# Optimization experiments

Hardware: AMD Instinct MI355X
Metric: run time of the kernel (lower is better)

Reference implementation:

```python
import jax, jax.numpy as jnp
import numpy as np

WS, OWS, NH = 16, 24, 2          # window size, overlap window size (=int(16*0.5)+16), num heads
PAD = (OWS - WS) // 2            # unfold padding = 4


def conv2d(x, w, b):
    kh, kw = w.shape[2], w.shape[3]
    out = jax.lax.conv_general_dilated(x, w, (1, 1), [(kh // 2, kh // 2), (kw // 2, kw // 2)],
                                       dimension_numbers=('NCHW', 'OIHW', 'NCHW'))
    return out + b[None, :, None, None]


def layer_norm(x, g, b, eps=1e-5):
    m = x.mean(-1, keepdims=True)
    v = ((x - m) ** 2).mean(-1, keepdims=True)
    return (x - m) * jax.lax.rsqrt(v + eps) * g + b


def stem(depth, cw1, cb1, cw2, cb2, cw3, cb3, cw4, cb4, in_g, in_b):
    # BasicConv(1->8,k3,relu) -> (8->16,k1,relu) -> (16->16,k3,relu) -> (16->32,k1) -> InstanceNorm2d(32,affine)
    y = jax.nn.relu(conv2d(depth, cw1, cb1))
    y = jax.nn.relu(conv2d(y, cw2, cb2))
    y = jax.nn.relu(conv2d(y, cw3, cb3))
    y = conv2d(y, cw4, cb4)
    m = y.mean((2, 3), keepdims=True)
    v = ((y - m) ** 2).mean((2, 3), keepdims=True)
    return (y - m) * jax.lax.rsqrt(v + 1e-5) * in_g[None, :, None, None] + in_b[None, :, None, None]


def ocab(xq, ykv, rpi, n1g, n1b, wq, bq, wkv, bkv, rpb, wp, bp, n2g, n2b, mw1, mb1, mw2, mb2):
    # Overlapping cross-attention block (HAT-style OCAB, cross variant: q from xq, kv from ykv).
    b, c, h, w = xq.shape
    x = xq.transpose(0, 2, 3, 1)   # b h w c
    y = ykv.transpose(0, 2, 3, 1)
    shortcut = x
    q = layer_norm(x, n1g, n1b) @ wq + bq          # b h w c
    kv = layer_norm(y, n1g, n1b) @ wkv + bkv       # b h w 2c
    nhw, nww = h // WS, w // WS
    # non-overlapping query windows: (b*nw, WS*WS, c)
    qw = q.reshape(b, nhw, WS, nww, WS, c).transpose(0, 1, 3, 2, 4, 5).reshape(b * nhw * nww, WS * WS, c)
    # overlapping kv windows via unfold (patch channel order = (channel, kh, kw), same as torch unfold)
    patches = jax.lax.conv_general_dilated_patches(kv.transpose(0, 3, 1, 2), (OWS, OWS), (WS, WS),
                                                   [(PAD, PAD), (PAD, PAD)])  # b, 2c*OWS*OWS, nhw, nww
    patches = patches.reshape(b, 2, c, OWS * OWS, nhw * nww).transpose(1, 0, 4, 3, 2).reshape(2, b * nhw * nww, OWS * OWS, c)
    k, v = patches[0], patches[1]
    d = c // NH
    qh = qw.reshape(-1, WS * WS, NH, d).transpose(0, 2, 1, 3) * (d ** -0.5)
    kh = k.reshape(-1, OWS * OWS, NH, d).transpose(0, 2, 1, 3)
    vh = v.reshape(-1, OWS * OWS, NH, d).transpose(0, 2, 1, 3)
    attn = jnp.einsum('whqd,whkd->whqk', qh, kh)
    attn = attn + rpb[rpi].transpose(2, 0, 1)[None]  # rel-pos bias -> [1, NH, WS*WS, OWS*OWS]
    attn = jax.nn.softmax(attn, axis=-1)
    out = jnp.einsum('whqk,whkd->whqd', attn, vh).transpose(0, 2, 1, 3).reshape(-1, WS * WS, c)
    # window reverse
    out = out.reshape(b, nhw, nww, WS, WS, c).transpose(0, 1, 3, 2, 4, 5).reshape(b, h, w, c)
    out = out @ wp + bp + shortcut
    out = out + (jax.nn.gelu(layer_norm(out, n2g, n2b) @ mw1 + mb1) @ mw2 + mb2)  # mlp_ratio=2
    return out.transpose(0, 3, 1, 2)


def setup_inputs():
    key = jax.random.key(0)
    ks = jax.random.split(key, 16)
    B, C, H, W = 1, 32, 256, 256
    s = 0.05
    return dict(
        x=jax.random.normal(ks[0], (B, C, H, W), jnp.float32),
        depth=jax.random.normal(ks[1], (B, 1, H, W), jnp.float32),
        rpi=jax.random.randint(ks[2], (WS * WS, OWS * OWS), 0, (WS + OWS - 1) ** 2),
        cw1=jax.random.normal(ks[3], (8, 1, 3, 3)) * s, cb1=jnp.zeros(8),
        cw2=jax.random.normal(ks[4], (16, 8, 1, 1)) * s, cb2=jnp.zeros(16),
        cw3=jax.random.normal(ks[5], (16, 16, 3, 3)) * s, cb3=jnp.zeros(16),
        cw4=jax.random.normal(ks[6], (32, 16, 1, 1)) * s, cb4=jnp.zeros(32),
        in_g=jnp.ones(32), in_b=jnp.zeros(32),
        n1g=jnp.ones(C), n1b=jnp.zeros(C),
        wq=jax.random.normal(ks[7], (C, C)) * s, bq=jnp.zeros(C),
        wkv=jax.random.normal(ks[8], (C, 2 * C)) * s, bkv=jnp.zeros(2 * C),
        rpb=jax.random.normal(ks[9], ((WS + OWS - 1) ** 2, NH)) * 0.02,
        wp=jax.random.normal(ks[10], (C, C)) * s, bp=jnp.zeros(C),
        n2g=jnp.ones(C), n2b=jnp.zeros(C),
        mw1=jax.random.normal(ks[11], (C, 2 * C)) * s, mb1=jnp.zeros(2 * C),
        mw2=jax.random.normal(ks[12], (2 * C, C)) * s, mb2=jnp.zeros(C),
    )


def reference(x, depth, rpi, cw1, cb1, cw2, cb2, cw3, cb3, cw4, cb4, in_g, in_b,
              n1g, n1b, wq, bq, wkv, bkv, rpb, wp, bp, n2g, n2b, mw1, mb1, mw2, mb2):
    f = stem(depth, cw1, cb1, cw2, cb2, cw3, cb3, cw4, cb4, in_g, in_b)
    a = (n1g, n1b, wq, bq, wkv, bkv, rpb, wp, bp, n2g, n2b, mw1, mb1, mw2, mb2)
    out1 = ocab(x, f, rpi, *a)   # shared OCAB weights, called twice with swapped roles
    out2 = ocab(f, x, rpi, *a)
    return out1 + out2 + x
```

## Files before the change

### kernel.cpp

```cpp
#include <hip/hip_runtime.h>
#include <hip/hip_bf16.h>

#define HW 65536
#define KPAD 584

typedef __attribute__((ext_vector_type(8))) short bf8;
typedef __attribute__((ext_vector_type(4))) float f4;

__device__ __forceinline__ unsigned short f2b(float x) {
  unsigned int u = __float_as_uint(x);
  unsigned int r = (u + 0x7fff + ((u >> 16) & 1)) >> 16;
  return (unsigned short)r;
}
__device__ __forceinline__ unsigned int pk2(float lo, float hi) {
  return (__float_as_uint(hi) & 0xffff0000u) | (__float_as_uint(lo) >> 16);
}

__device__ __forceinline__ void stem_front_body(
    int bx, int t, const float* __restrict__ depth,
    const float* __restrict__ cw1, const float* __restrict__ cb1,
    const float* __restrict__ cw2, const float* __restrict__ cb2,
    float* __restrict__ t2) {
  int p = bx * 256 + t;
  int y = p >> 8, x = p & 255;
  float in9[9];
#pragma unroll
  for (int ky = 0; ky < 3; ky++)
#pragma unroll
    for (int kx = 0; kx < 3; kx++) {
      int yy = y + ky - 1, xx = x + kx - 1;
      bool ok = ((unsigned)yy < 256u) && ((unsigned)xx < 256u);
      in9[ky*3+kx] = ok ? depth[yy*256+xx] : 0.f;
    }
  float t1[8];
#pragma unroll
  for (int o = 0; o < 8; o++) {
    float s = cb1[o];
#pragma unroll
    for (int i = 0; i < 9; i++) s += in9[i] * cw1[o*9+i];
    t1[o] = fmaxf(s, 0.f);
  }
#pragma unroll
  for (int o = 0; o < 16; o++) {
    float s = cb2[o];
#pragma unroll
    for (int ci = 0; ci < 8; ci++) s += t1[ci] * cw2[o*8+ci];
    t2[o*HW + p] = fmaxf(s, 0.f);
  }
}

__device__ __forceinline__ void bias_body(
    int bx, int t, const int* __restrict__ rpi,
    const float* __restrict__ rpb, float* __restrict__ biasT) {
  int idx = bx*256 + t;
  int hd = idx / 147456;
  int rem = idx - hd*147456;
  int qt = rem / 9216;
  int r2 = rem - qt*9216;
  int kb = r2 >> 6;
  int q16 = (r2 >> 2) & 15;
  int r = r2 & 3;
  int key = kb*4 + r;
  int qq = qt*16 + q16;
  biasT[idx] = rpb[rpi[qq*576 + key]*2 + hd] - 8.0f;
}

__device__ __forceinline__ void lnmm_body(
    int slab, int bx, int t,
    float* ws, float* gs, float* bs, float* b2s, float* as, float* bbs,
    const float* __restrict__ x, const float* __restrict__ t4,
    const float* __restrict__ part,
    const float* __restrict__ ig, const float* __restrict__ ib,
    const float* __restrict__ n1g, const float* __restrict__ n1b,
    const float* __restrict__ wq, const float* __restrict__ bq,
    const float* __restrict__ wkv, const float* __restrict__ bkv,
    float* q1, float* kv1, float* q2, float* kv2) {
  const float* src; const float* wm; const float* bo; float* dst;
  int wstride, coff; bool apply_in;
  switch (slab) {
    default:
    case 0: src=x;  wm=wq;  bo=bq;  dst=q1;         wstride=32; coff=0;  apply_in=false; break;
    case 1: src=t4; wm=wkv; bo=bkv; dst=kv1;        wstride=64; coff=0;  apply_in=true;  break;
    case 2: src=t4; wm=wkv; bo=bkv; dst=kv1+32*HW;  wstride=64; coff=32; apply_in=true;  break;
    case 3: src=t4; wm=wq;  bo=bq;  dst=q2;         wstride=32; coff=0;  apply_in=true;  break;
    case 4: src=x;  wm=wkv; bo=bkv; dst=kv2;        wstride=64; coff=0;  apply_in=false; break;
    case 5: src=x;  wm=wkv; bo=bkv; dst=kv2+32*HW;  wstride=64; coff=32; apply_in=false; break;
  }
  for (int i = t; i < 1024; i += 256) ws[i] = wm[(i>>5)*wstride + coff + (i&31)];
  if (t < 32) {
    gs[t] = n1g[t]; bs[t] = n1b[t]; b2s[t] = bo[coff+t];
    if (apply_in) {
      float s = 0.f, ss = 0.f;
#pragma unroll
      for (int k = 0; k < 16; k++) { s += part[t*16+k]; ss += part[512 + t*16+k]; }
      float m = s * (1.f/65536.f);
      float var = ss * (1.f/65536.f) - m*m;
      float a = rsqrtf(var + 1e-5f) * ig[t];
      as[t] = a; bbs[t] = ib[t] - m*a;
    }
  }
  __syncthreads();
  int p = bx*256 + t;
  float v[32]; float s = 0.f;
  if (apply_in) {
#pragma unroll
    for (int c = 0; c < 32; c++) { v[c] = src[c*HW+p]*as[c] + bbs[c]; s += v[c]; }
  } else {
#pragma unroll
    for (int c = 0; c < 32; c++) { v[c] = src[c*HW+p]; s += v[c]; }
  }
  float m = s * 0.03125f;
  float ss = 0.f;
#pragma unroll
  for (int c = 0; c < 32; c++) { float d = v[c]-m; ss += d*d; }
  float rs = rsqrtf(ss*0.03125f + 1e-5f);
  float acc[32];
#pragma unroll
  for (int j = 0; j < 32; j++) acc[j] = b2s[j];
#pragma unroll
  for (int c = 0; c < 32; c++) {
    float ln = (v[c]-m)*rs*gs[c] + bs[c];
    const float4* w4 = (const float4*)&ws[c*32];
#pragma unroll
    for (int j4 = 0; j4 < 8; j4++) {
      float4 w = w4[j4];
      acc[j4*4+0] += ln*w.x; acc[j4*4+1] += ln*w.y;
      acc[j4*4+2] += ln*w.z; acc[j4*4+3] += ln*w.w;
    }
  }
#pragma unroll
  for (int j = 0; j < 32; j++) dst[j*HW+p] = acc[j];
}

__global__ __launch_bounds__(256) void k_misc(
    const float* __restrict__ depth,
    const float* __restrict__ cw1, const float* __restrict__ cb1,
    const float* __restrict__ cw2, const float* __restrict__ cb2,
    float* __restrict__ t2,
    const int* __restrict__ rpi, const float* __restrict__ rpb, float* __restrict__ biasT,
    const float* __restrict__ x, const float* __restrict__ t4, const float* __restrict__ part,
    const float* __restrict__ ig, const float* __restrict__ ib,
    const float* __restrict__ n1g, const float* __restrict__ n1b,
    const float* __restrict__ wq, const float* __restrict__ bq,
    const float* __restrict__ wkv, const float* __restrict__ bkv,
    float* q1, float* kv1, float* q2, float* kv2) {
  __shared__ __align__(16) float ws[1024];
  __shared__ float gs[32], bs[32], b2s[32], as[32], bbs[32];
  int role = blockIdx.y, t = threadIdx.x, bx = blockIdx.x;
  if (role == 0) { if (bx < 256) stem_front_body(bx, t, depth, cw1, cb1, cw2, cb2, t2); return; }
  if (role == 1) { bias_body(bx, t, rpi, rpb, biasT); return; }
  if (bx >= 256) return;
  int slab = (role == 2) ? 0 : role + 1;
  lnmm_body(slab, bx, t, ws, gs, bs, b2s, as, bbs,
            x, t4, part, ig, ib, n1g, n1b, wq, bq, wkv, bkv, q1, kv1, q2, kv2);
}

__global__ __launch_bounds__(256) void k_lnmm3(
    const float* __restrict__ x, const float* __restrict__ t4, const float* __restrict__ part,
    const float* __restrict__ ig, const float* __restrict__ ib,
    const float* __restrict__ n1g, const float* __restrict__ n1b,
    const float* __restrict__ wq, const float* __restrict__ bq,
    const float* __restrict__ wkv, const float* __restrict__ bkv,
    float* q1, float* kv1, float* q2, float* kv2, int ybase) {
  __shared__ __align__(16) float ws[1024];
  __shared__ float gs[32], bs[32], b2s[32], as[32], bbs[32];
  lnmm_body(ybase + blockIdx.y, blockIdx.x, threadIdx.x, ws, gs, bs, b2s, as, bbs,
            x, t4, part, ig, ib, n1g, n1b, wq, bq, wkv, bkv, q1, kv1, q2, kv2);
}

__global__ __launch_bounds__(256) void k_conv3(
    const float* __restrict__ t2, const float* __restrict__ cw3,
    const float* __restrict__ cb3, float* __restrict__ t3) {
  int t = threadIdx.x;
  int p = blockIdx.x*256 + t;
  int og = blockIdx.y;
  int y = p >> 8, x = p & 255;
  float acc[4];
#pragma unroll
  for (int o = 0; o < 4; o++) acc[o] = cb3[og*4+o];
#pragma unroll 1
  for (int tap = 0; tap < 9; tap++) {
    int ky = tap/3 - 1, kx = tap - (tap/3)*3 - 1;
    int yy = y+ky, xx = x+kx;
    bool ok = ((unsigned)yy < 256u) && ((unsigned)xx < 256u);
    int pp = yy*256+xx;
#pragma unroll
    for (int ci = 0; ci < 16; ci++) {
      float v = ok ? t2[ci*HW+pp] : 0.f;
#pragma unroll
      for (int o = 0; o < 4; o++)
        acc[o] += v * cw3[(og*4+o)*144 + ci*9 + tap];
    }
  }
#pragma unroll
  for (int o = 0; o < 4; o++) t3[(og*4+o)*HW+p] = fmaxf(acc[o], 0.f);
}

__global__ __launch_bounds__(256) void k_conv4(
    const float* __restrict__ t3, const float* __restrict__ cw4,
    const float* __restrict__ cb4, float* __restrict__ t4) {
  int t = threadIdx.x;
  int p = blockIdx.x*256 + t;
  float v[16];
#pragma unroll
  for (int ci = 0; ci < 16; ci++) v[ci] = t3[ci*HW+p];
#pragma unroll
  for (int o = 0; o < 32; o++) {
    float s = cb4[o];
#pragma unroll
    for (int ci = 0; ci < 16; ci++) s += v[ci]*cw4[o*16+ci];
    t4[o*HW+p] = s;
  }
}

__global__ __launch_bounds__(256) void k_instats1(const float* __restrict__ t4,
                                                  float* __restrict__ part) {
  int c = blockIdx.x >> 4, seg = blockIdx.x & 15;
  const float4* src = (const float4*)(t4 + c*HW + seg*4096);
  float s = 0.f, ss = 0.f;
  for (int i = threadIdx.x; i < 1024; i += 256) {
    float4 v = src[i];
    s  += v.x + v.y + v.z + v.w;
    ss += v.x*v.x + v.y*v.y + v.z*v.z + v.w*v.w;
  }
#pragma unroll
  for (int off = 32; off > 0; off >>= 1) {
    s  += __shfl_down(s, off, 64);
    ss += __shfl_down(ss, off, 64);
  }
  __shared__ float sh[8];
  int wid = threadIdx.x >> 6;
  if ((threadIdx.x & 63) == 0) { sh[wid] = s; sh[4+wid] = ss; }
  __syncthreads();
  if (threadIdx.x == 0) {
    part[blockIdx.x]       = sh[0]+sh[1]+sh[2]+sh[3];
    part[512 + blockIdx.x] = sh[4]+sh[5]+sh[6]+sh[7];
  }
}

__global__ __launch_bounds__(256) void k_attn(
    const float* __restrict__ qA, const float* __restrict__ kvA, float* __restrict__ aoA,
    const float* __restrict__ qB, const float* __restrict__ kvB, float* __restrict__ aoB,
    const float* __restrict__ biasT) {
  __shared__ __align__(16) unsigned short Qs[256*16];
  __shared__ __align__(16) unsigned short Ks[576*16];
  __shared__ __align__(16) unsigned short Vt[16*KPAD];

  const float* q  = blockIdx.y ? qB  : qA;
  const float* kv = blockIdx.y ? kvB : kvA;
  float* ao       = blockIdx.y ? aoB : aoA;

  int wi = blockIdx.x >> 1, hd = blockIdx.x & 1;
  int wy = wi >> 4, wx = wi & 15;
  int t = threadIdx.x;
  int by = wy*16 - 4, bx = wx*16 - 4;
  int kbase = hd*16*HW, vbase = (32 + hd*16)*HW;

  {
    int qy = wy*16 + (t >> 4), qx = wx*16 + (t & 15);
    int p = qy*256 + qx;
    unsigned short tmp[16];
#pragma unroll
    for (int i = 0; i < 16; i++) tmp[i] = f2b(q[(hd*16+i)*HW + p] * 0.25f);
    *(uint4*)&Qs[t*16]     = *(uint4*)&tmp[0];
    *(uint4*)&Qs[t*16 + 8] = *(uint4*)&tmp[8];
  }
  for (int e = t; e < 576; e += 256) {
    int dy = e / 24, dx = e - dy*24;
    int yy = by + dy, xx = bx + dx;
    bool ok = ((unsigned)yy < 256u) && ((unsigned)xx < 256u);
    int pp = yy*256 + xx;
    int off = e & 31;
    int ppos = ((off & 12) << 1) + ((off >> 4) << 2) + (off & 3);
    int vcol = (e & ~31) + ppos;
    unsigned short tk[16];
#pragma unroll
    for (int i = 0; i < 16; i++) {
      float kvl = ok ? kv[kbase + i*HW + pp] : 0.f;
      float vvl = ok ? kv[vbase + i*HW + pp] : 0.f;
      tk[i] = f2b(kvl);
      Vt[i*KPAD + vcol] = f2b(vvl);
    }
    *(uint4*)&Ks[e*16]     = *(uint4*)&tk[0];
    *(uint4*)&Ks[e*16 + 8] = *(uint4*)&tk[8];
  }
  __syncthreads();

  int wave = t >> 6, lane = t & 63;
  int quad = lane >> 4, l16 = lane & 15;
  const bf8 zero8 = {0,0,0,0,0,0,0,0};

#pragma unroll 1
  for (int pp2 = 0; pp2 < 2; pp2++) {
    int qta = wave*4 + pp2*2, qtb = qta + 1;
    bf8 qfa = zero8, qfb = zero8;
    if (quad < 2) {
      qfa = *(const bf8*)&Qs[(qta*16 + l16)*16 + quad*8];
      qfb = *(const bf8*)&Qs[(qtb*16 + l16)*16 + quad*8];
    }
    f4 oa = {0.f,0.f,0.f,0.f}, ob = {0.f,0.f,0.f,0.f};
    float la = 0.f, lb = 0.f;
    const float* bba = biasT + (hd*16 + qta)*9216 + quad*64 + l16*4;
    const float* bbb = biasT + (hd*16 + qtb)*9216 + quad*64 + l16*4;
    f4 ba0 = *(const f4*)&bba[0];
    f4 ba1 = *(const f4*)&bba[256];
    f4 bb0 = *(const f4*)&bbb[0];
    f4 bb1 = *(const f4*)&bbb[256];

#pragma unroll 2
    for (int kt2 = 0; kt2 < 18; kt2++) {
      int k0 = kt2 * 32;
      f4 na0 = *(const f4*)&bba[(k0+32)*16];
      f4 na1 = *(const f4*)&bba[(k0+48)*16];
      f4 nb0 = *(const f4*)&bbb[(k0+32)*16];
      f4 nb1 = *(const f4*)&bbb[(k0+48)*16];
      bf8 kf0 = zero8, kf1 = zero8;
      if (quad < 2) {
        kf0 = *(const bf8*)&Ks[(k0 + l16)*16 + quad*8];
        kf1 = *(const bf8*)&Ks[(k0 + 16 + l16)*16 + quad*8];
      }
      f4 sa0 = __builtin_amdgcn_mfma_f32_16x16x32_bf16(kf0, qfa, ba0, 0, 0, 0);
      f4 sa1 = __builtin_amdgcn_mfma_f32_16x16x32_bf16(kf1, qfa, ba1, 0, 0, 0);
      f4 sb0 = __builtin_amdgcn_mfma_f32_16x16x32_bf16(kf0, qfb, bb0, 0, 0, 0);
      f4 sb1 = __builtin_amdgcn_mfma_f32_16x16x32_bf16(kf1, qfb, bb1, 0, 0, 0);
      float pa0[4], pa1[4], pb0[4], pb1[4];
#pragma unroll
      for (int r = 0; r < 4; r++) {
        pa0[r] = __expf(sa0[r]); pa1[r] = __expf(sa1[r]);
        pb0[r] = __expf(sb0[r]); pb1[r] = __expf(sb1[r]);
        la += pa0[r] + pa1[r];
        lb += pb0[r] + pb1[r];
      }
      union { unsigned int u[4]; bf8 v; } Pa, Pb;
      Pa.u[0] = pk2(pa0[0], pa0[1]); Pa.u[1] = pk2(pa0[2], pa0[3]);
      Pa.u[2] = pk2(pa1[0], pa1[1]); Pa.u[3] = pk2(pa1[2], pa1[3]);
      Pb.u[0] = pk2(pb0[0], pb0[1]); Pb.u[1] = pk2(pb0[2], pb0[3]);
      Pb.u[2] = pk2(pb1[0], pb1[1]); Pb.u[3] = pk2(pb1[2], pb1[3]);
      bf8 vf = *(const bf8*)&Vt[l16*KPAD + k0 + quad*8];
      oa = __builtin_amdgcn_mfma_f32_16x16x32_bf16(Pa.v, vf, oa, 0, 0, 0);
      ob = __builtin_amdgcn_mfma_f32_16x16x32_bf16(Pb.v, vf, ob, 0, 0, 0);
      ba0 = na0; ba1 = na1; bb0 = nb0; bb1 = nb1;
    }
    la += __shfl_xor(la, 16, 64); la += __shfl_xor(la, 32, 64);
    lb += __shfl_xor(lb, 16, 64); lb += __shfl_xor(lb, 32, 64);
#pragma unroll
    for (int r = 0; r < 4; r++) {
      float lva = __shfl(la, quad*4 + r, 64);
      float lvb = __shfl(lb, quad*4 + r, 64);
      int qwa = qta*16 + quad*4 + r;
      int qwb = qtb*16 + quad*4 + r;
      ao[(hd*16 + l16)*HW + (wy*16 + (qwa >> 4))*256 + wx*16 + (qwa & 15)] = oa[r] / lva;
      ao[(hd*16 + l16)*HW + (wy*16 + (qwb >> 4))*256 + wx*16 + (qwb & 15)] = ob[r] / lvb;
    }
  }
}

__global__ __launch_bounds__(256) void k_projmlp(
    const float* __restrict__ ao1, const float* __restrict__ ao2,
    const float* __restrict__ x, const float* __restrict__ t4,
    const float* __restrict__ part,
    const float* __restrict__ ig, const float* __restrict__ ib,
    const float* __restrict__ wp, const float* __restrict__ bp,
    const float* __restrict__ n2g, const float* __restrict__ n2b,
    const float* __restrict__ mw1, const float* __restrict__ mb1,
    const float* __restrict__ mw2, const float* __restrict__ mb2,
    float* __restrict__ o1, float* __restrict__ o2, int obase) {
  int oc = blockIdx.y + obase;
  const float* ao = oc ? ao2 : ao1;
  float* dst      = oc ? o2  : o1;
  __shared__ __align__(16) float wps[1024];
  __shared__ __align__(16) float w1s[2048];
  __shared__ __align__(16) float w2s[2048];
  __shared__ float bps[32], b1s[64], b2s[32], gs[32], bs[32], as[32], bbs[32];
  int t = threadIdx.x;
  for (int i = t; i < 1024; i += 256) wps[i] = wp[i];
  for (int i = t; i < 2048; i += 256) { w1s[i] = mw1[i]; w2s[i] = mw2[i]; }
  if (t < 64) b1s[t] = mb1[t];
  if (t < 32) {
    bps[t] = bp[t]; b2s[t] = mb2[t]; gs[t] = n2g[t]; bs[t] = n2b[t];
    float s = 0.f, ss = 0.f;
#pragma unroll
    for (int k = 0; k < 16; k++) { s += part[t*16+k]; ss += part[512 + t*16+k]; }
    float m = s * (1.f/65536.f);
    float var = ss * (1.f/65536.f) - m*m;
    float a = rsqrtf(var + 1e-5f) * ig[t];
    as[t] = a; bbs[t] = ib[t] - m*a;
  }
  __syncthreads();
  int p = blockIdx.x*256 + t;
  float acc[32];
#pragma unroll
  for (int j = 0; j < 32; j++) acc[j] = bps[j];
#pragma unroll
  for (int c = 0; c < 32; c++) {
    float vc = ao[c*HW+p];
    const float4* w4 = (const float4*)&wps[c*32];
#pragma unroll
    for (int j4 = 0; j4 < 8; j4++) {
      float4 w = w4[j4];
      acc[j4*4+0] += vc*w.x; acc[j4*4+1] += vc*w.y;
      acc[j4*4+2] += vc*w.z; acc[j4*4+3] += vc*w.w;
    }
  }
  if (oc == 0) {
#pragma unroll
    for (int j = 0; j < 32; j++) acc[j] += x[j*HW+p];
  } else {
#pragma unroll
    for (int j = 0; j < 32; j++) acc[j] += t4[j*HW+p]*as[j] + bbs[j];
  }
  float s = 0.f;
#pragma unroll
  for (int j = 0; j < 32; j++) s += acc[j];
  float m = s * 0.03125f;
  float ss = 0.f;
#pragma unroll
  for (int j = 0; j < 32; j++) { float d = acc[j]-m; ss += d*d; }
  float rs = rsqrtf(ss*0.03125f + 1e-5f);
  float r[32];
#pragma unroll
  for (int j = 0; j < 32; j++) r[j] = b2s[j];
#pragma unroll 1
  for (int half = 0; half < 2; half++) {
    float h[32];
#pragma unroll
    for (int k = 0; k < 32; k++) h[k] = b1s[half*32 + k];
#pragma unroll
    for (int c = 0; c < 32; c++) {
      float ln = (acc[c] - m) * rs * gs[c] + bs[c];
      const float4* w4 = (const float4*)&w1s[c*64 + half*32];
#pragma unroll
      for (int k4 = 0; k4 < 8; k4++) {
        float4 w = w4[k4];
        h[k4*4+0] += ln*w.x; h[k4*4+1] += ln*w.y; h[k4*4+2] += ln*w.z; h[k4*4+3] += ln*w.w;
      }
    }
#pragma unroll
    for (int k = 0; k < 32; k++) {
      float xx = h[k];
      float u = 0.7978845608f * (xx + 0.044715f*xx*xx*xx);
      float th = 1.f - 2.f/(1.f + __expf(2.f*u));
      h[k] = 0.5f * xx * (1.f + th);
    }
#pragma unroll
    for (int k = 0; k < 32; k++) {
      float hk = h[k];
      const float4* w4 = (const float4*)&w2s[(half*32 + k)*32];
#pragma unroll
      for (int j4 = 0; j4 < 8; j4++) {
        float4 w = w4[j4];
        r[j4*4+0] += hk*w.x; r[j4*4+1] += hk*w.y; r[j4*4+2] += hk*w.z; r[j4*4+3] += hk*w.w;
      }
    }
  }
#pragma unroll
  for (int j = 0; j < 32; j++) dst[j*HW + p] = acc[j] + r[j];
}

__global__ __launch_bounds__(256) void k_final(
    const float* o1, const float* __restrict__ o2,
    const float* __restrict__ x, float* out) {
  int i = blockIdx.x*256 + threadIdx.x;
  float4 a = ((const float4*)o1)[i];
  float4 b = ((const float4*)o2)[i];
  float4 c = ((const float4*)x)[i];
  float4 r;
  r.x = a.x + b.x + c.x; r.y = a.y + b.y + c.y;
  r.z = a.z + b.z + c.z; r.w = a.w + b.w + c.w;
  ((float4*)out)[i] = r;
}

extern "C" void kernel_launch(void* const* d_in, const int* in_sizes, int n_in,
                              void* d_out, int out_size, void* d_ws, size_t ws_size,
                              hipStream_t stream) {
  const float* x    = (const float*)d_in[0];
  const float* depth= (const float*)d_in[1];
  const int*   rpi  = (const int*)d_in[2];
  const float* cw1  = (const float*)d_in[3],  *cb1 = (const float*)d_in[4];
  const float* cw2  = (const float*)d_in[5],  *cb2 = (const float*)d_in[6];
  const float* cw3  = (const float*)d_in[7],  *cb3 = (const float*)d_in[8];
  const float* cw4  = (const float*)d_in[9],  *cb4 = (const float*)d_in[10];
  const float* in_g = (const float*)d_in[11], *in_b = (const float*)d_in[12];
  const float* n1g  = (const float*)d_in[13], *n1b = (const float*)d_in[14];
  const float* wq   = (const float*)d_in[15], *bq  = (const float*)d_in[16];
  const float* wkv  = (const float*)d_in[17], *bkv = (const float*)d_in[18];
  const float* rpb  = (const float*)d_in[19];
  const float* wp   = (const float*)d_in[20], *bp  = (const float*)d_in[21];
  const float* n2g  = (const float*)d_in[22], *n2b = (const float*)d_in[23];
  const float* mw1  = (const float*)d_in[24], *mb1 = (const float*)d_in[25];
  const float* mw2  = (const float*)d_in[26], *mb2 = (const float*)d_in[27];

  float* W   = (float*)d_ws;
  float* o1  = (float*)d_out;

  bool big = ws_size >= (size_t)85100000;

  if (big) {
    float* t4    = W;
    float* q1    = W + 2097152;
    float* q2    = W + 4194304;
    float* kv1   = W + 6291456;
    float* kv2   = W + 10485760;
    float* ao1   = W + 14680064;
    float* ao2   = W + 16777216;
    float* o2    = W + 18874368;
    float* biasT = W + 20971520;
    float* part  = W + 21266432;
    float* t2 = ao1, *t3 = q2;

    k_misc   <<<dim3(1152,5), 256, 0, stream>>>(depth, cw1, cb1, cw2, cb2, t2,
                                                rpi, rpb, biasT,
                                                x, t4, part, in_g, in_b, n1g, n1b,
                                                wq, bq, wkv, bkv, q1, kv1, q2, kv2);
    k_conv3  <<<dim3(256,4), 256, 0, stream>>>(t2, cw3, cb3, t3);
    k_conv4  <<<256, 256, 0, stream>>>(t3, cw4, cb4, t4);
    k_instats1<<<512, 256, 0, stream>>>(t4, part);
    k_lnmm3  <<<dim3(256,3), 256, 0, stream>>>(x, t4, part, in_g, in_b, n1g, n1b,
                                               wq, bq, wkv, bkv, q1, kv1, q2, kv2, 1);
    k_attn   <<<dim3(512,2), 256, 0, stream>>>(q1, kv1, ao1, q2, kv2, ao2, biasT);
    k_projmlp<<<dim3(256,2), 256, 0, stream>>>(ao1, ao2, x, t4, part, in_g, in_b,
                                               wp, bp, n2g, n2b, mw1, mb1, mw2, mb2,
                                               o1, o2, 0);
    k_final  <<<2048, 256, 0, stream>>>(o1, o2, x, o1);
  } else {
    float* t4    = W;
    float* q1    = W + 2097152;
    float* kv1   = W + 4194304;
    float* ao1   = W + 8388608;
    float* o2    = W + 10485760;
    float* biasT = W + 12582912;
    float* part  = W + 12877824;
    float* t2 = ao1, *t3 = o2;

    k_misc   <<<dim3(1152,2), 256, 0, stream>>>(depth, cw1, cb1, cw2, cb2, t2,
                                                rpi, rpb, biasT,
                                                x, t4, part, in_g, in_b, n1g, n1b,
                                                wq, bq, wkv, bkv, q1, kv1, q1, kv1);
    k_conv3  <<<dim3(256,4), 256, 0, stream>>>(t2, cw3, cb3, t3);
    k_conv4  <<<256, 256, 0, stream>>>(t3, cw4, cb4, t4);
    k_instats1<<<512, 256, 0, stream>>>(t4, part);
    k_lnmm3  <<<dim3(256,3), 256, 0, stream>>>(x, t4, part, in_g, in_b, n1g, n1b,
                                               wq, bq, wkv, bkv, q1, kv1, q1, kv1, 0);
    k_attn   <<<dim3(512,1), 256, 0, stream>>>(q1, kv1, ao1, q1, kv1, ao1, biasT);
    k_projmlp<<<dim3(256,1), 256, 0, stream>>>(ao1, ao1, x, t4, part, in_g, in_b,
                                               wp, bp, n2g, n2b, mw1, mb1, mw2, mb2,
                                               o1, o2, 0);
    k_lnmm3  <<<dim3(256,3), 256, 0, stream>>>(x, t4, part, in_g, in_b, n1g, n1b,
                                               wq, bq, wkv, bkv, q1, kv1, q1, kv1, 3);
    k_attn   <<<dim3(512,1), 256, 0, stream>>>(q1, kv1, ao1, q1, kv1, ao1, biasT);
    k_projmlp<<<dim3(256,1), 256, 0, stream>>>(ao1, ao1, x, t4, part, in_g, in_b,
                                               wp, bp, n2g, n2b, mw1, mb1, mw2, mb2,
                                               o1, o2, 1);
    k_final  <<<2048, 256, 0, stream>>>(o1, o2, x, o1);
  }
}
```

Baseline: 296.5 us.

## Split LN-matmul and conv4 into narrower slabs, restructure attention loop with exp2

```diff
diff --git a/kernel.cpp b/kernel.cpp
--- a/kernel.cpp
+++ b/kernel.cpp
@@ -15,6 +15,7 @@
 __device__ __forceinline__ unsigned int pk2(float lo, float hi) {
   return (__float_as_uint(hi) & 0xffff0000u) | (__float_as_uint(lo) >> 16);
 }
+__device__ __forceinline__ float ex2(float x) { return __builtin_amdgcn_exp2f(x); }
 
 __device__ __forceinline__ void stem_front_body(
     int bx, int t, const float* __restrict__ depth,
@@ -62,11 +63,11 @@
   int r = r2 & 3;
   int key = kb*4 + r;
   int qq = qt*16 + q16;
-  biasT[idx] = rpb[rpi[qq*576 + key]*2 + hd] - 8.0f;
-}
-
-__device__ __forceinline__ void lnmm_body(
-    int slab, int bx, int t,
+  biasT[idx] = (rpb[rpi[qq*576 + key]*2 + hd] - 8.0f) * 1.44269504f;
+}
+
+__device__ __forceinline__ void lnmm16_body(
+    int role, int bx, int t,
     float* ws, float* gs, float* bs, float* b2s, float* as, float* bbs,
     const float* __restrict__ x, const float* __restrict__ t4,
     const float* __restrict__ part,
@@ -75,21 +76,25 @@
     const float* __restrict__ wq, const float* __restrict__ bq,
     const float* __restrict__ wkv, const float* __restrict__ bkv,
     float* q1, float* kv1, float* q2, float* kv2) {
-  const float* src; const float* wm; const float* bo; float* dst;
-  int wstride, coff; bool apply_in;
-  switch (slab) {
+  const float *src, *wm, *bo; float* dst;
+  int wstride, wcol; bool ain;
+  if (role < 6) { src = x;  ain = false; } else { src = t4; ain = true; }
+  switch (role) {
     default:
-    case 0: src=x;  wm=wq;  bo=bq;  dst=q1;         wstride=32; coff=0;  apply_in=false; break;
-    case 1: src=t4; wm=wkv; bo=bkv; dst=kv1;        wstride=64; coff=0;  apply_in=true;  break;
-    case 2: src=t4; wm=wkv; bo=bkv; dst=kv1+32*HW;  wstride=64; coff=32; apply_in=true;  break;
-    case 3: src=t4; wm=wq;  bo=bq;  dst=q2;         wstride=32; coff=0;  apply_in=true;  break;
-    case 4: src=x;  wm=wkv; bo=bkv; dst=kv2;        wstride=64; coff=0;  apply_in=false; break;
-    case 5: src=x;  wm=wkv; bo=bkv; dst=kv2+32*HW;  wstride=64; coff=32; apply_in=false; break;
-  }
-  for (int i = t; i < 1024; i += 256) ws[i] = wm[(i>>5)*wstride + coff + (i&31)];
+    case 0:  wm=wq;  wstride=32; wcol=0;  bo=bq;  dst=q1;               break;
+    case 1:  wm=wq;  wstride=32; wcol=16; bo=bq;  dst=q1+16*HW;         break;
+    case 2: case 3: case 4: case 5:
+             wm=wkv; wstride=64; wcol=16*(role-2); bo=bkv; dst=kv2+16*(role-2)*HW; break;
+    case 6:  wm=wq;  wstride=32; wcol=0;  bo=bq;  dst=q2;               break;
+    case 7:  wm=wq;  wstride=32; wcol=16; bo=bq;  dst=q2+16*HW;         break;
+    case 8: case 9: case 10: case 11:
+             wm=wkv; wstride=64; wcol=16*(role-8); bo=bkv; dst=kv1+16*(role-8)*HW; break;
+  }
+  for (int i = t; i < 512; i += 256) ws[i] = wm[(i>>4)*wstride + wcol + (i&15)];
+  if (t < 16) b2s[t] = bo[wcol + t];
   if (t < 32) {
-    gs[t] = n1g[t]; bs[t] = n1b[t]; b2s[t] = bo[coff+t];
-    if (apply_in) {
+    gs[t] = n1g[t]; bs[t] = n1b[t];
+    if (ain) {
       float s = 0.f, ss = 0.f;
 #pragma unroll
       for (int k = 0; k < 16; k++) { s += part[t*16+k]; ss += part[512 + t*16+k]; }
@@ -102,7 +107,7 @@
   __syncthreads();
   int p = bx*256 + t;
   float v[32]; float s = 0.f;
-  if (apply_in) {
+  if (ain) {
 #pragma unroll
     for (int c = 0; c < 32; c++) { v[c] = src[c*HW+p]*as[c] + bbs[c]; s += v[c]; }
   } else {
@@ -114,22 +119,22 @@
 #pragma unroll
   for (int c = 0; c < 32; c++) { float d = v[c]-m; ss += d*d; }
   float rs = rsqrtf(ss*0.03125f + 1e-5f);
-  float acc[32];
-#pragma unroll
-  for (int j = 0; j < 32; j++) acc[j] = b2s[j];
+  float acc[16];
+#pragma unroll
+  for (int j = 0; j < 16; j++) acc[j] = b2s[j];
 #pragma unroll
   for (int c = 0; c < 32; c++) {
     float ln = (v[c]-m)*rs*gs[c] + bs[c];
-    const float4* w4 = (const float4*)&ws[c*32];
-#pragma unroll
-    for (int j4 = 0; j4 < 8; j4++) {
+    const float4* w4 = (const float4*)&ws[c*16];
+#pragma unroll
+    for (int j4 = 0; j4 < 4; j4++) {
       float4 w = w4[j4];
       acc[j4*4+0] += ln*w.x; acc[j4*4+1] += ln*w.y;
       acc[j4*4+2] += ln*w.z; acc[j4*4+3] += ln*w.w;
     }
   }
 #pragma unroll
-  for (int j = 0; j < 32; j++) dst[j*HW+p] = acc[j];
+  for (int j = 0; j < 16; j++) dst[j*HW+p] = acc[j];
 }
 
 __global__ __launch_bounds__(256) void k_misc(
@@ -144,28 +149,27 @@
     const float* __restrict__ wq, const float* __restrict__ bq,
     const float* __restrict__ wkv, const float* __restrict__ bkv,
     float* q1, float* kv1, float* q2, float* kv2) {
-  __shared__ __align__(16) float ws[1024];
-  __shared__ float gs[32], bs[32], b2s[32], as[32], bbs[32];
+  __shared__ __align__(16) float ws[512];
+  __shared__ float gs[32], bs[32], b2s[16], as[32], bbs[32];
   int role = blockIdx.y, t = threadIdx.x, bx = blockIdx.x;
   if (role == 0) { if (bx < 256) stem_front_body(bx, t, depth, cw1, cb1, cw2, cb2, t2); return; }
   if (role == 1) { bias_body(bx, t, rpi, rpb, biasT); return; }
   if (bx >= 256) return;
-  int slab = (role == 2) ? 0 : role + 1;
-  lnmm_body(slab, bx, t, ws, gs, bs, b2s, as, bbs,
-            x, t4, part, ig, ib, n1g, n1b, wq, bq, wkv, bkv, q1, kv1, q2, kv2);
-}
-
-__global__ __launch_bounds__(256) void k_lnmm3(
+  lnmm16_body(role - 2, bx, t, ws, gs, bs, b2s, as, bbs,
+              x, t4, part, ig, ib, n1g, n1b, wq, bq, wkv, bkv, q1, kv1, q2, kv2);
+}
+
+__global__ __launch_bounds__(256) void k_lnmmB(
     const float* __restrict__ x, const float* __restrict__ t4, const float* __restrict__ part,
     const float* __restrict__ ig, const float* __restrict__ ib,
     const float* __restrict__ n1g, const float* __restrict__ n1b,
     const float* __restrict__ wq, const float* __restrict__ bq,
     const float* __restrict__ wkv, const float* __restrict__ bkv,
     float* q1, float* kv1, float* q2, float* kv2, int ybase) {
-  __shared__ __align__(16) float ws[1024];
-  __shared__ float gs[32], bs[32], b2s[32], as[32], bbs[32];
-  lnmm_body(ybase + blockIdx.y, blockIdx.x, threadIdx.x, ws, gs, bs, b2s, as, bbs,
-            x, t4, part, ig, ib, n1g, n1b, wq, bq, wkv, bkv, q1, kv1, q2, kv2);
+  __shared__ __align__(16) float ws[512];
+  __shared__ float gs[32], bs[32], b2s[16], as[32], bbs[32];
+  lnmm16_body(ybase + blockIdx.y, blockIdx.x, threadIdx.x, ws, gs, bs, b2s, as, bbs,
+              x, t4, part, ig, ib, n1g, n1b, wq, bq, wkv, bkv, q1, kv1, q2, kv2);
 }
 
 __global__ __launch_bounds__(256) void k_conv3(
@@ -201,15 +205,17 @@
     const float* __restrict__ cb4, float* __restrict__ t4) {
   int t = threadIdx.x;
   int p = blockIdx.x*256 + t;
+  int og = blockIdx.y;
   float v[16];
 #pragma unroll
   for (int ci = 0; ci < 16; ci++) v[ci] = t3[ci*HW+p];
 #pragma unroll
-  for (int o = 0; o < 32; o++) {
-    float s = cb4[o];
-#pragma unroll
-    for (int ci = 0; ci < 16; ci++) s += v[ci]*cw4[o*16+ci];
-    t4[o*HW+p] = s;
+  for (int o = 0; o < 8; o++) {
+    int oo = og*8 + o;
+    float s = cb4[oo];
+#pragma unroll
+    for (int ci = 0; ci < 16; ci++) s += v[ci]*cw4[oo*16+ci];
+    t4[oo*HW+p] = s;
   }
 }
 
@@ -238,7 +244,7 @@
   }
 }
 
-__global__ __launch_bounds__(256) void k_attn(
+__global__ __launch_bounds__(256, 3) void k_attn(
     const float* __restrict__ qA, const float* __restrict__ kvA, float* __restrict__ aoA,
     const float* __restrict__ qB, const float* __restrict__ kvB, float* __restrict__ aoB,
     const float* __restrict__ biasT) {
@@ -250,7 +256,9 @@
   const float* kv = blockIdx.y ? kvB : kvA;
   float* ao       = blockIdx.y ? aoB : aoA;
 
-  int wi = blockIdx.x >> 1, hd = blockIdx.x & 1;
+  int id = blockIdx.x;
+  int lin = ((id & 7) << 6) | (id >> 3);
+  int wi = lin >> 1, hd = lin & 1;
   int wy = wi >> 4, wx = wi & 15;
   int t = threadIdx.x;
   int by = wy*16 - 4, bx = wx*16 - 4;
@@ -261,7 +269,7 @@
     int p = qy*256 + qx;
     unsigned short tmp[16];
 #pragma unroll
-    for (int i = 0; i < 16; i++) tmp[i] = f2b(q[(hd*16+i)*HW + p] * 0.25f);
+    for (int i = 0; i < 16; i++) tmp[i] = f2b(q[(hd*16+i)*HW + p] * 0.360673503f);
     *(uint4*)&Qs[t*16]     = *(uint4*)&tmp[0];
     *(uint4*)&Qs[t*16 + 8] = *(uint4*)&tmp[8];
   }
@@ -290,67 +298,61 @@
   int quad = lane >> 4, l16 = lane & 15;
   const bf8 zero8 = {0,0,0,0,0,0,0,0};
 
-#pragma unroll 1
-  for (int pp2 = 0; pp2 < 2; pp2++) {
-    int qta = wave*4 + pp2*2, qtb = qta + 1;
-    bf8 qfa = zero8, qfb = zero8;
+  bf8 qf[4];
+  f4 oacc[4];
+  float lr[4];
+  const float* bb[4];
+#pragma unroll
+  for (int qi = 0; qi < 4; qi++) {
+    int qt = wave*4 + qi;
+    qf[qi] = zero8;
+    if (quad < 2) qf[qi] = *(const bf8*)&Qs[(qt*16 + l16)*16 + quad*8];
+    oacc[qi] = (f4){0.f,0.f,0.f,0.f};
+    lr[qi] = 0.f;
+    bb[qi] = biasT + (hd*16 + qt)*9216 + quad*64 + l16*4;
+  }
+
+#pragma unroll 2
+  for (int kt2 = 0; kt2 < 18; kt2++) {
+    int k0 = kt2 * 32;
+    bf8 kf0 = zero8, kf1 = zero8;
     if (quad < 2) {
-      qfa = *(const bf8*)&Qs[(qta*16 + l16)*16 + quad*8];
-      qfb = *(const bf8*)&Qs[(qtb*16 + l16)*16 + quad*8];
-    }
-    f4 oa = {0.f,0.f,0.f,0.f}, ob = {0.f,0.f,0.f,0.f};
-    float la = 0.f, lb = 0.f;
-    const float* bba = biasT + (hd*16 + qta)*9216 + quad*64 + l16*4;
-    const float* bbb = biasT + (hd*16 + qtb)*9216 + quad*64 + l16*4;
-    f4 ba0 = *(const f4*)&bba[0];
-    f4 ba1 = *(const f4*)&bba[256];
-    f4 bb0 = *(const f4*)&bbb[0];
-    f4 bb1 = *(const f4*)&bbb[256];
-
-#pragma unroll 2
-    for (int kt2 = 0; kt2 < 18; kt2++) {
-      int k0 = kt2 * 32;
-      f4 na0 = *(const f4*)&bba[(k0+32)*16];
-      f4 na1 = *(const f4*)&bba[(k0+48)*16];
-      f4 nb0 = *(const f4*)&bbb[(k0+32)*16];
-      f4 nb1 = *(const f4*)&bbb[(k0+48)*16];
-      bf8 kf0 = zero8, kf1 = zero8;
-      if (quad < 2) {
-        kf0 = *(const bf8*)&Ks[(k0 + l16)*16 + quad*8];
-        kf1 = *(const bf8*)&Ks[(k0 + 16 + l16)*16 + quad*8];
+      kf0 = *(const bf8*)&Ks[(k0 + l16)*16 + quad*8];
+      kf1 = *(const bf8*)&Ks[(k0 + 16 + l16)*16 + quad*8];
+    }
+    bf8 vf = *(const bf8*)&Vt[l16*KPAD + k0 + quad*8];
+#pragma unroll
+    for (int qi = 0; qi < 4; qi++) {
+      f4 b0 = *(const f4*)&bb[qi][k0*16];
+      f4 b1 = *(const f4*)&bb[qi][(k0+16)*16];
+      f4 s0 = __builtin_amdgcn_mfma_f32_16x16x32_bf16(kf0, qf[qi], b0, 0, 0, 0);
+      f4 s1 = __builtin_amdgcn_mfma_f32_16x16x32_bf16(kf1, qf[qi], b1, 0, 0, 0);
+      float p0[4], p1[4];
+#pragma unroll
+      for (int r = 0; r < 4; r++) {
+        p0[r] = ex2(s0[r]);
+        p1[r] = ex2(s1[r]);
+        lr[qi] += p0[r] + p1[r];
       }
-      f4 sa0 = __builtin_amdgcn_mfma_f32_16x16x32_bf16(kf0, qfa, ba0, 0, 0, 0);
-      f4 sa1 = __builtin_amdgcn_mfma_f32_16x16x32_bf16(kf1, qfa, ba1, 0, 0, 0);
-      f4 sb0 = __builtin_amdgcn_mfma_f32_16x16x32_bf16(kf0, qfb, bb0, 0, 0, 0);
-      f4 sb1 = __builtin_amdgcn_mfma_f32_16x16x32_bf16(kf1, qfb, bb1, 0, 0, 0);
-      float pa0[4], pa1[4], pb0[4], pb1[4];
-#pragma unroll
-      for (int r = 0; r < 4; r++) {
-        pa0[r] = __expf(sa0[r]); pa1[r] = __expf(sa1[r]);
-        pb0[r] = __expf(sb0[r]); pb1[r] = __expf(sb1[r]);
-        la += pa0[r] + pa1[r];
-        lb += pb0[r] + pb1[r];
-      }
-      union { unsigned int u[4]; bf8 v; } Pa, Pb;
-      Pa.u[0] = pk2(pa0[0], pa0[1]); Pa.u[1] = pk2(pa0[2], pa0[3]);
-      Pa.u[2] = pk2(pa1[0], pa1[1]); Pa.u[3] = pk2(pa1[2], pa1[3]);
-      Pb.u[0] = pk2(pb0[0], pb0[1]); Pb.u[1] = pk2(pb0[2], pb0[3]);
-      Pb.u[2] = pk2(pb1[0], pb1[1]); Pb.u[3] = pk2(pb1[2], pb1[3]);
-      bf8 vf = *(const bf8*)&Vt[l16*KPAD + k0 + quad*8];
-      oa = __builtin_amdgcn_mfma_f32_16x16x32_bf16(Pa.v, vf, oa, 0, 0, 0);
-      ob = __builtin_amdgcn_mfma_f32_16x16x32_bf16(Pb.v, vf, ob, 0, 0, 0);
-      ba0 = na0; ba1 = na1; bb0 = nb0; bb1 = nb1;
-    }
-    la += __shfl_xor(la, 16, 64); la += __shfl_xor(la, 32, 64);
-    lb += __shfl_xor(lb, 16, 64); lb += __shfl_xor(lb, 32, 64);
+      union { unsigned int u[4]; bf8 v; } P;
+      P.u[0] = pk2(p0[0], p0[1]); P.u[1] = pk2(p0[2], p0[3]);
+      P.u[2] = pk2(p1[0], p1[1]); P.u[3] = pk2(p1[2], p1[3]);
+      oacc[qi] = __builtin_amdgcn_mfma_f32_16x16x32_bf16(P.v, vf, oacc[qi], 0, 0, 0);
+    }
+  }
+#pragma unroll
+  for (int qi = 0; qi < 4; qi++) {
+    lr[qi] += __shfl_xor(lr[qi], 16, 64);
+    lr[qi] += __shfl_xor(lr[qi], 32, 64);
+  }
+#pragma unroll
+  for (int qi = 0; qi < 4; qi++) {
+    int qt = wave*4 + qi;
 #pragma unroll
     for (int r = 0; r < 4; r++) {
-      float lva = __shfl(la, quad*4 + r, 64);
-      float lvb = __shfl(lb, quad*4 + r, 64);
-      int qwa = qta*16 + quad*4 + r;
-      int qwb = qtb*16 + quad*4 + r;
-      ao[(hd*16 + l16)*HW + (wy*16 + (qwa >> 4))*256 + wx*16 + (qwa & 15)] = oa[r] / lva;
-      ao[(hd*16 + l16)*HW + (wy*16 + (qwb >> 4))*256 + wx*16 + (qwb & 15)] = ob[r] / lvb;
+      float lv = __shfl(lr[qi], quad*4 + r, 64);
+      int qw = qt*16 + quad*4 + r;
+      ao[(hd*16 + l16)*HW + (wy*16 + (qw >> 4))*256 + wx*16 + (qw & 15)] = oacc[qi][r] / lv;
     }
   }
 }
@@ -508,15 +510,15 @@
     float* part  = W + 21266432;
     float* t2 = ao1, *t3 = q2;
 
-    k_misc   <<<dim3(1152,5), 256, 0, stream>>>(depth, cw1, cb1, cw2, cb2, t2,
+    k_misc   <<<dim3(1152,8), 256, 0, stream>>>(depth, cw1, cb1, cw2, cb2, t2,
                                                 rpi, rpb, biasT,
                                                 x, t4, part, in_g, in_b, n1g, n1b,
                                                 wq, bq, wkv, bkv, q1, kv1, q2, kv2);
     k_conv3  <<<dim3(256,4), 256, 0, stream>>>(t2, cw3, cb3, t3);
-    k_conv4  <<<256, 256, 0, stream>>>(t3, cw4, cb4, t4);
+    k_conv4  <<<dim3(256,4), 256, 0, stream>>>(t3, cw4, cb4, t4);
     k_instats1<<<512, 256, 0, stream>>>(t4, part);
-    k_lnmm3  <<<dim3(256,3), 256, 0, stream>>>(x, t4, part, in_g, in_b, n1g, n1b,
-                                               wq, bq, wkv, bkv, q1, kv1, q2, kv2, 1);
+    k_lnmmB  <<<dim3(256,6), 256, 0, stream>>>(x, t4, part, in_g, in_b, n1g, n1b,
+                                               wq, bq, wkv, bkv, q1, kv1, q2, kv2, 6);
     k_attn   <<<dim3(512,2), 256, 0, stream>>>(q1, kv1, ao1, q2, kv2, ao2, biasT);
     k_projmlp<<<dim3(256,2), 256, 0, stream>>>(ao1, ao2, x, t4, part, in_g, in_b,
                                                wp, bp, n2g, n2b, mw1, mb1, mw2, mb2,
@@ -532,21 +534,21 @@
     float* part  = W + 12877824;
     float* t2 = ao1, *t3 = o2;
 
-    k_misc   <<<dim3(1152,2), 256, 0, stream>>>(depth, cw1, cb1, cw2, cb2, t2,
+    k_misc   <<<dim3(1152,4), 256, 0, stream>>>(depth, cw1, cb1, cw2, cb2, t2,
                                                 rpi, rpb, biasT,
                                                 x, t4, part, in_g, in_b, n1g, n1b,
                                                 wq, bq, wkv, bkv, q1, kv1, q1, kv1);
     k_conv3  <<<dim3(256,4), 256, 0, stream>>>(t2, cw3, cb3, t3);
-    k_conv4  <<<256, 256, 0, stream>>>(t3, cw4, cb4, t4);
+    k_conv4  <<<dim3(256,4), 256, 0, stream>>>(t3, cw4, cb4, t4);
     k_instats1<<<512, 256, 0, stream>>>(t4, part);
-    k_lnmm3  <<<dim3(256,3), 256, 0, stream>>>(x, t4, part, in_g, in_b, n1g, n1b,
-                                               wq, bq, wkv, bkv, q1, kv1, q1, kv1, 0);
+    k_lnmmB  <<<dim3(256,4), 256, 0, stream>>>(x, t4, part, in_g, in_b, n1g, n1b,
+                                               wq, bq, wkv, bkv, q1, kv1, q1, kv1, 8);
     k_attn   <<<dim3(512,1), 256, 0, stream>>>(q1, kv1, ao1, q1, kv1, ao1, biasT);
     k_projmlp<<<dim3(256,1), 256, 0, stream>>>(ao1, ao1, x, t4, part, in_g, in_b,
                                                wp, bp, n2g, n2b, mw1, mb1, mw2, mb2,
                                                o1, o2, 0);
-    k_lnmm3  <<<dim3(256,3), 256, 0, stream>>>(x, t4, part, in_g, in_b, n1g, n1b,
-                                               wq, bq, wkv, bkv, q1, kv1, q1, kv1, 3);
+    k_lnmmB  <<<dim3(256,6), 256, 0, stream>>>(x, t4, part, in_g, in_b, n1g, n1b,
+                                               wq, bq, wkv, bkv, q1, kv1, q1, kv1, 2);
     k_attn   <<<dim3(512,1), 256, 0, stream>>>(q1, kv1, ao1, q1, kv1, ao1, biasT);
     k_projmlp<<<dim3(256,1), 256, 0, stream>>>(ao1, ao1, x, t4, part, in_g, in_b,
                                                wp, bp, n2g, n2b, mw1, mb1, mw2, mb2,
```

After: 279.7 us. 1.06x faster.
